# Kernel optimization log

Hardware: AMD Instinct MI355X
Metric: run time of the kernel (lower is better)

Reference implementation:

```python
import jax, jax.numpy as jnp
import numpy as np

EMBED_DIM = 1024
NUM_HEADS = 16
HEAD_DIM = EMBED_DIM // NUM_HEADS  # used only for the softmax scale


def setup_inputs() -> dict:
    key = jax.random.key(0)
    k_x, k_wqkv, k_bqkv, k_wo, k_bo = jax.random.split(key, 5)
    bound_qkv = 1.0 / np.sqrt(EMBED_DIM)
    return {
        "x": jax.random.normal(k_x, (4, 2048, EMBED_DIM), dtype=jnp.float32),
        "W_qkv": jax.random.uniform(k_wqkv, (EMBED_DIM, 3 * EMBED_DIM), jnp.float32, -bound_qkv, bound_qkv),
        "b_qkv": jax.random.uniform(k_bqkv, (3 * EMBED_DIM,), jnp.float32, -bound_qkv, bound_qkv),
        "W_out": jax.random.uniform(k_wo, (EMBED_DIM, EMBED_DIM), jnp.float32, -bound_qkv, bound_qkv),
        "b_out": jax.random.uniform(k_bo, (EMBED_DIM,), jnp.float32, -bound_qkv, bound_qkv),
    }


def reference(x, W_qkv, b_qkv, W_out, b_out):
    # fused QKV projection: [B,S,3E]
    qkv = jnp.einsum("bse,ef->bsf", x, W_qkv) + b_qkv
    q, k, v = jnp.split(qkv, 3, axis=-1)  # each [B,S,E]
    scale = 1.0 / jnp.sqrt(jnp.float32(HEAD_DIM))
    # NOTE: no head reshape — attention over full embed_dim, scale uses head_dim
    scores = jnp.einsum("bqe,bke->bqk", q, k) * scale  # [B,S,S]
    attn = jax.nn.softmax(scores, axis=-1)
    context = jnp.einsum("bqk,bke->bqe", attn, v)  # [B,S,E]
    return jnp.einsum("bse,ef->bsf", context, W_out) + b_out
```

## Files before the change

kernel.cpp:

```cpp
#include <hip/hip_runtime.h>

typedef unsigned short u16;
typedef __bf16   bf16x8 __attribute__((ext_vector_type(8)));
typedef float    f32x4  __attribute__((ext_vector_type(4)));
typedef unsigned short u16x4 __attribute__((ext_vector_type(4)));
typedef unsigned short u16x8 __attribute__((ext_vector_type(8)));

__device__ inline float bf2f(u16 u) { return __uint_as_float(((unsigned int)u) << 16); }
__device__ inline u16 f2bf(float f) {
    unsigned int u = __float_as_uint(f);
    u += 0x7FFF + ((u >> 16) & 1);
    return (u16)(u >> 16);
}

__device__ inline void gl2lds16(const u16* g, u16* l) {
    __builtin_amdgcn_global_load_lds(
        (const __attribute__((address_space(1))) void*)g,
        (__attribute__((address_space(3))) void*)l, 16, 0, 0);
}

__global__ __launch_bounds__(256)
void sniff_zero(const u16* __restrict__ x, int* __restrict__ flag,
                float* __restrict__ sums) {
    sums[blockIdx.x * 256 + threadIdx.x] = 0.0f;
    if (blockIdx.x == 0 && threadIdx.x < 64) {
        const int lane = threadIdx.x;
        const unsigned idx = lane * 131072u + 65536u;
        const u16 u = x[idx];
        const int e = (u >> 7) & 0xFF;
        const unsigned long long b = __ballot(e >= 100 && e <= 140);
        if (lane == 0) flag[0] = (__popcll(b) >= 48) ? 0 : 1;
    }
}

__global__ __launch_bounds__(256)
void convx_biases(const void* __restrict__ x, u16* __restrict__ xbf,
                  const void* __restrict__ b1, const void* __restrict__ b2,
                  u16* __restrict__ o1, u16* __restrict__ o2,
                  const int* __restrict__ flagp) {
    const int f = *flagp;
    if (blockIdx.x < 8192) {
        const long i = ((long)blockIdx.x * 256 + threadIdx.x) * 4;
        if (f) {
            f32x4 v = *(const f32x4*)((const float*)x + i);
            u16x4 o; o[0] = f2bf(v[0]); o[1] = f2bf(v[1]); o[2] = f2bf(v[2]); o[3] = f2bf(v[3]);
            *(u16x4*)(xbf + i) = o;
        } else {
            *(u16x4*)(xbf + i) = *(const u16x4*)((const u16*)x + i);
        }
    } else {
        const int i = (blockIdx.x - 8192) * 256 + threadIdx.x;
        if (i < 3072) o1[i] = f ? f2bf(((const float*)b1)[i]) : ((const u16*)b1)[i];
        else { const int j = i - 3072;
               o2[j] = f ? f2bf(((const float*)b2)[j]) : ((const u16*)b2)[j]; }
    }
}

__global__ __launch_bounds__(256)
void transpose_w(const void* __restrict__ Wqkv, u16* __restrict__ WqkvT,
                 const void* __restrict__ Wout, u16* __restrict__ WoutT,
                 const int* __restrict__ flagp)
{
    const void* in; u16* out; long inStride, outStride;
    if (blockIdx.z == 0) { in = Wqkv; out = WqkvT; inStride = 3072; outStride = 1024; }
    else { if (blockIdx.x >= 32) return;
           in = Wout; out = WoutT; inStride = 1024; outStride = 1024; }
    __shared__ u16 t[32][36];
    const int isF32 = *flagp;
    const int tid = threadIdx.x;
    const long r0 = (long)blockIdx.y * 32;
    const long c0 = (long)blockIdx.x * 32;
    const int r  = tid >> 3;
    const int c4 = (tid & 7) * 4;
    const long base = (r0 + r) * inStride + c0 + c4;
    u16x4 v;
    if (isF32) {
        f32x4 f = *(const f32x4*)((const float*)in + base);
        v[0] = f2bf(f[0]); v[1] = f2bf(f[1]); v[2] = f2bf(f[2]); v[3] = f2bf(f[3]);
    } else {
        v = *(const u16x4*)((const u16*)in + base);
    }
    t[r][c4 + 0] = v[0]; t[r][c4 + 1] = v[1]; t[r][c4 + 2] = v[2]; t[r][c4 + 3] = v[3];
    __syncthreads();
    u16x4 o;
    o[0] = t[c4 + 0][r]; o[1] = t[c4 + 1][r]; o[2] = t[c4 + 2][r]; o[3] = t[c4 + 3][r];
    *(u16x4*)&out[(c0 + r) * outStride + r0 + c4] = o;
}

template <int GM, int GN, int WM, int WN>
__device__ __forceinline__ void kloop(
    const u16* __restrict__ A, const u16* __restrict__ Bt,
    int K, long lda, long ldb, long m0, long n0,
    u16* __restrict__ As, u16* __restrict__ Bs, f32x4 (&acc)[WM][WN])
{
    constexpr int BM = GM * WM * 16;
    constexpr int BN = GN * WN * 16;
    constexpr int IA = BM / 32;
    constexpr int IB = BN / 32;
    const int tid  = threadIdx.x;
    const int lane = tid & 63;
    const int wave = tid >> 6;
    const int sr   = tid >> 3;
    const int qg0  = (tid & 7) ^ (sr & 7);
    const u16* pa[IA]; const u16* pb[IB];
    u16* la[IA]; u16* lb[IB];
#pragma unroll
    for (int i = 0; i < IA; ++i) {
        pa[i] = A + (m0 + i * 32 + sr) * lda + qg0 * 8;
        la[i] = As + (i * 256 + wave * 64) * 8;
    }
#pragma unroll
    for (int i = 0; i < IB; ++i) {
        pb[i] = Bt + (n0 + i * 32 + sr) * ldb + qg0 * 8;
        lb[i] = Bs + (i * 256 + wave * 64) * 8;
    }
    const int wm = (wave / GN) * (WM * 16);
    const int wn = (wave % GN) * (WN * 16);
    const int lr = lane & 15;
    const int hk = lane >> 4;
    int aoff[WM][2], boff[WN][2];
#pragma unroll
    for (int i = 0; i < WM; ++i) {
        const int row = wm + i * 16 + lr, r7 = row & 7;
        aoff[i][0] = row * 64 + ((hk     ^ r7) * 8);
        aoff[i][1] = row * 64 + (((4+hk) ^ r7) * 8);
    }
#pragma unroll
    for (int j = 0; j < WN; ++j) {
        const int row = wn + j * 16 + lr, r7 = row & 7;
        boff[j][0] = row * 64 + ((hk     ^ r7) * 8);
        boff[j][1] = row * 64 + (((4+hk) ^ r7) * 8);
    }
    for (int kt = 0; kt < K; kt += 64) {
#pragma unroll
        for (int i = 0; i < IA; ++i) { gl2lds16(pa[i], la[i]); pa[i] += 64; }
#pragma unroll
        for (int i = 0; i < IB; ++i) { gl2lds16(pb[i], lb[i]); pb[i] += 64; }
        __syncthreads();
#pragma unroll
        for (int ks = 0; ks < 2; ++ks) {
            bf16x8 af[WM], bf[WN];
#pragma unroll
            for (int i = 0; i < WM; ++i) af[i] = *(const bf16x8*)&As[aoff[i][ks]];
#pragma unroll
            for (int j = 0; j < WN; ++j) bf[j] = *(const bf16x8*)&Bs[boff[j][ks]];
#pragma unroll
            for (int i = 0; i < WM; ++i)
#pragma unroll
                for (int j = 0; j < WN; ++j)
                    acc[i][j] = __builtin_amdgcn_mfma_f32_16x16x32_bf16(af[i], bf[j], acc[i][j], 0, 0, 0);
        }
        __syncthreads();
    }
}

template <int WM, int WN, typename F>
__device__ __forceinline__ void epi_bf16(u16* __restrict__ Sw, u16* __restrict__ C,
    long ldc, long gm0, long gn0, int lane, F f)
{
    const int lr = lane & 15, hk = lane >> 4;
#pragma unroll
    for (int i = 0; i < WM; ++i)
#pragma unroll
        for (int j = 0; j < WN; ++j)
#pragma unroll
            for (int r = 0; r < 4; ++r)
                Sw[(i*16 + hk*4 + r) * (WN*16) + j*16 + lr] = f2bf(f(i, j, r));
    asm volatile("s_waitcnt lgkmcnt(0)" ::: "memory");
    constexpr int LPR = WN * 2;
    constexpr int RPI = 64 / LPR;
    const int rl = lane / LPR, c8 = (lane % LPR) * 8;
#pragma unroll
    for (int t = 0; t < (WM*16) / RPI; ++t) {
        const int row = t * RPI + rl;
        u16x8 v8 = *(const u16x8*)&Sw[row * (WN*16) + c8];
        *(u16x8*)&C[(gm0 + row) * ldc + gn0 + c8] = v8;
    }
}

template <int WM, int WN, typename F>
__device__ __forceinline__ void epi_f32(float* __restrict__ Sw, float* __restrict__ C,
    long ldc, long gm0, long gn0, int lane, F f)
{
    const int lr = lane & 15, hk = lane >> 4;
#pragma unroll
    for (int jh = 0; jh < 2; ++jh) {
#pragma unroll
        for (int i = 0; i < WM; ++i)
#pragma unroll
            for (int jj = 0; jj < WN/2; ++jj)
#pragma unroll
                for (int r = 0; r < 4; ++r)
                    Sw[(i*16 + hk*4 + r) * (WN*8) + jj*16 + lr] = f(i, jh*(WN/2) + jj, r);
        asm volatile("s_waitcnt lgkmcnt(0)" ::: "memory");
        constexpr int LPR = WN * 2;
        constexpr int RPI = 64 / LPR;
        const int rl = lane / LPR, c4 = (lane % LPR) * 4;
#pragma unroll
        for (int t = 0; t < (WM*16) / RPI; ++t) {
            const int row = t * RPI + rl;
            f32x4 v4 = *(const f32x4*)&Sw[row * (WN*8) + c4];
            *(f32x4*)&C[(gm0 + row) * ldc + gn0 + jh*(WN*8) + c4] = v4;
        }
        asm volatile("s_waitcnt lgkmcnt(0)" ::: "memory");
    }
}

__global__ __launch_bounds__(256, 4)
void gemm_qkv(const u16* __restrict__ A, const u16* __restrict__ Bt,
              u16* __restrict__ C, const u16* __restrict__ bias)
{
    __shared__ __align__(16) u16 S[256 * 64];
    const long m0 = (long)blockIdx.y * 128, n0 = (long)blockIdx.x * 128;
    f32x4 acc[4][4] = {};
    kloop<2, 2, 4, 4>(A, Bt, 1024, 1024L, 1024L, m0, n0, S, S + 128*64, acc);
    const int lane = threadIdx.x & 63, wave = threadIdx.x >> 6;
    const int wm = (wave >> 1) * 64, wn = (wave & 1) * 64;
    const int lr = lane & 15;
    float bj[4];
#pragma unroll
    for (int j = 0; j < 4; ++j) bj[j] = bf2f(bias[n0 + wn + j*16 + lr]);
    epi_bf16<4, 4>(S + wave * 4096, C, 3072L, m0 + wm, n0 + wn, lane,
        [&](int i, int j, int r) { return acc[i][j][r] + bj[j]; });
}

__global__ __launch_bounds__(256, 4)
void gemm_phase2(const u16* __restrict__ QKV, u16* __restrict__ P,
                 const u16* __restrict__ WoutT, u16* __restrict__ VWT,
                 float* __restrict__ sums)
{
    __shared__ __align__(16) u16 S[256 * 64];
    const int z = blockIdx.z;
    const u16 *Ap, *Bp; u16* Cp; long lda, ldb, ldc, m0, n0;
    bool doExp; float* srow = nullptr;
    if (z < 4) {
        const long zb = (long)z * 2048 * 3072;
        Ap = QKV + zb; Bp = QKV + 1024 + zb;
        Cp = P + (long)z * 2048 * 2048;
        lda = 3072; ldb = 3072; ldc = 2048;
        m0 = (long)blockIdx.y * 128; n0 = (long)blockIdx.x * 128;
        doExp = true; srow = sums + z * 2048;
    } else {
        const int vb = (z - 4) * 2 + (blockIdx.y >> 3);
        Ap = WoutT; lda = 1024;
        Bp = QKV + 2048 + (long)vb * 2048 * 3072; ldb = 3072;
        Cp = VWT + (long)vb * 1024 * 2048; ldc = 2048;
        m0 = (long)(blockIdx.y & 7) * 128; n0 = (long)blockIdx.x * 128;
        doExp = false;
    }
    f32x4 acc[4][4] = {};
    kloop<2, 2, 4, 4>(Ap, Bp, 1024, lda, ldb, m0, n0, S, S + 128*64, acc);
    const int lane = threadIdx.x & 63, wave = threadIdx.x >> 6;
    const int wm = (wave >> 1) * 64, wn = (wave & 1) * 64;
    const int lr = lane & 15, hk = lane >> 4;
    u16* Sw = S + wave * 4096;
    if (doExp) {
#pragma unroll
        for (int i = 0; i < 4; ++i)
#pragma unroll
            for (int r = 0; r < 4; ++r) {
                const int lrow = i*16 + hk*4 + r;
                float s = 0.0f;
#pragma unroll
                for (int j = 0; j < 4; ++j) {
                    const float e = __expf(acc[i][j][r] * 0.125f);
                    Sw[lrow * 64 + j*16 + lr] = f2bf(e);
                    s += e;
                }
                s += __shfl_xor(s, 1); s += __shfl_xor(s, 2);
                s += __shfl_xor(s, 4); s += __shfl_xor(s, 8);
                if (lr == 0) atomicAdd(&srow[m0 + wm + lrow], s);
            }
        asm volatile("s_waitcnt lgkmcnt(0)" ::: "memory");
        const int rl = lane >> 3, c8 = (lane & 7) * 8;
#pragma unroll
        for (int t = 0; t < 8; ++t) {
            const int row = t * 8 + rl;
            u16x8 v8 = *(const u16x8*)&Sw[row * 64 + c8];
            *(u16x8*)&Cp[(m0 + wm + row) * ldc + n0 + wn + c8] = v8;
        }
    } else {
        epi_bf16<4, 4>(Sw, Cp, ldc, m0 + wm, n0 + wn, lane,
            [&](int i, int j, int r) { return acc[i][j][r]; });
    }
}

__global__ __launch_bounds__(256, 4)
void gemm_final(const u16* __restrict__ P, const u16* __restrict__ VWT,
                void* __restrict__ out, const u16* __restrict__ bias,
                const float* __restrict__ sums, const int* __restrict__ flagp)
{
    __shared__ __align__(16) u16 S[256 * 64];
    const int outF32 = *flagp;
    const long bz = blockIdx.z;
    const long m0 = (long)blockIdx.y * 128, n0 = (long)blockIdx.x * 128;
    f32x4 acc[4][4] = {};
    kloop<2, 2, 4, 4>(P + bz * 2048 * 2048, VWT + bz * 1024 * 2048,
                      2048, 2048L, 2048L, m0, n0, S, S + 128*64, acc);
    const int lane = threadIdx.x & 63, wave = threadIdx.x >> 6;
    const int wm = (wave >> 1) * 64, wn = (wave & 1) * 64;
    const int lr = lane & 15, hk = lane >> 4;
    float inv[4][4], bj[4];
#pragma unroll
    for (int i = 0; i < 4; ++i)
#pragma unroll
        for (int r = 0; r < 4; ++r)
            inv[i][r] = 1.0f / sums[bz * 2048 + m0 + wm + i*16 + hk*4 + r];
#pragma unroll
    for (int j = 0; j < 4; ++j) bj[j] = bf2f(bias[n0 + wn + j*16 + lr]);
    if (outF32) {
        float* Co = (float*)out + bz * 2048 * 1024;
        epi_f32<4, 4>((float*)S + wave * 2048, Co, 1024L, m0 + wm, n0 + wn, lane,
            [&](int i, int j, int r) { return acc[i][j][r] * inv[i][r] + bj[j]; });
    } else {
        u16* Co = (u16*)out + bz * 2048 * 1024;
        epi_bf16<4, 4>(S + wave * 4096, Co, 1024L, m0 + wm, n0 + wn, lane,
            [&](int i, int j, int r) { return acc[i][j][r] * inv[i][r] + bj[j]; });
    }
}

extern "C" void kernel_launch(void* const* d_in, const int* in_sizes, int n_in,
                              void* d_out, int out_size, void* d_ws, size_t ws_size,
                              hipStream_t stream)
{
    const void* x    = d_in[0];
    const void* Wqkv = d_in[1];
    const void* bqkv = d_in[2];
    const void* Wout = d_in[3];
    const void* bout = d_in[4];
    char* ws = (char*)d_ws;

    u16*   xbf   = (u16*)(ws);
    u16*   WqkvT = (u16*)(ws + 16777216);
    u16*   P     = (u16*)(ws);
    u16*   QKV   = (u16*)(ws + 33554432);
    u16*   VWT   = (u16*)(ws + 83886080);
    u16*   WoutT = (u16*)(ws + 100663296);
    u16*   bqkvc = (u16*)(ws + 102760448);
    u16*   boutc = (u16*)(ws + 102766592);
    int*   flag  = (int*)(ws + 102768640);
    float* sums  = (float*)(ws + 102772736);

    dim3 blk(256);

    sniff_zero<<<32, blk, 0, stream>>>((const u16*)x, flag, sums);
    convx_biases<<<8208, blk, 0, stream>>>(x, xbf, bqkv, bout, bqkvc, boutc, flag);
    transpose_w<<<dim3(96, 32, 2), blk, 0, stream>>>(Wqkv, WqkvT, Wout, WoutT, flag);

    gemm_qkv<<<dim3(24, 64, 1), blk, 0, stream>>>(xbf, WqkvT, QKV, bqkvc);

    gemm_phase2<<<dim3(16, 16, 6), blk, 0, stream>>>(QKV, P, WoutT, VWT, sums);

    gemm_final<<<dim3(8, 16, 4), blk, 0, stream>>>(P, VWT, d_out, boutc, sums, flag);
}
```

Measured before the change: 267.3 us.

## Use 256x256 tiles with 8-wave four-phase pipelined k-loop for QKV and phase2 GEMMs

Replaces the 128x128, 4-wave GEMM kernels for the QKV projection and the scores/V·Wout stage with 256x256 tiles on 512-thread blocks. The new k-loop splits each 64-wide k-step into four quarter phases that interleave direct global-to-LDS loads of the next tile with MFMA work, and raises wave priority during the MFMAs. The goal is better operand reuse per byte loaded and hiding load latency. The cost is 128 KB of LDS per block and fewer blocks per CU, and a 256-row tile grid that may fill the GPU's CUs less evenly.

```diff
diff --git a/kernel.cpp b/kernel.cpp
--- a/kernel.cpp
+++ b/kernel.cpp
@@ -206,30 +206,152 @@
     }
 }
 
-__global__ __launch_bounds__(256, 4)
-void gemm_qkv(const u16* __restrict__ A, const u16* __restrict__ Bt,
-              u16* __restrict__ C, const u16* __restrict__ bias)
-{
-    __shared__ __align__(16) u16 S[256 * 64];
-    const long m0 = (long)blockIdx.y * 128, n0 = (long)blockIdx.x * 128;
-    f32x4 acc[4][4] = {};
-    kloop<2, 2, 4, 4>(A, Bt, 1024, 1024L, 1024L, m0, n0, S, S + 128*64, acc);
+template<int MH, int NH, typename FI>
+__device__ __forceinline__ void phase256(const u16* Ab, const u16* Bb,
+    int aB0, int aB1, int bB0, int bB1, f32x4 (&acc)[2][2][4][2], FI issue)
+{
+    bf16x8 af[2][4], bv[2][2];
+#pragma unroll
+    for (int i = 0; i < 4; ++i) {
+        af[0][i] = *(const bf16x8*)&Ab[aB0 + MH*8192 + i*1024];
+        af[1][i] = *(const bf16x8*)&Ab[aB1 + MH*8192 + i*1024];
+    }
+#pragma unroll
+    for (int j = 0; j < 2; ++j) {
+        bv[0][j] = *(const bf16x8*)&Bb[bB0 + NH*8192 + j*1024];
+        bv[1][j] = *(const bf16x8*)&Bb[bB1 + NH*8192 + j*1024];
+    }
+    issue();
+    __builtin_amdgcn_s_barrier();
+    asm volatile("s_waitcnt lgkmcnt(0)" ::: "memory");
+    __builtin_amdgcn_s_setprio(1);
+#pragma unroll
+    for (int ks = 0; ks < 2; ++ks)
+#pragma unroll
+        for (int i = 0; i < 4; ++i)
+#pragma unroll
+            for (int j = 0; j < 2; ++j)
+                acc[MH][NH][i][j] = __builtin_amdgcn_mfma_f32_16x16x32_bf16(
+                    af[ks][i], bv[ks][j], acc[MH][NH][i][j], 0, 0, 0);
+    __builtin_amdgcn_s_setprio(0);
+}
+
+__device__ __forceinline__ void kloop256(
+    const u16* __restrict__ A, const u16* __restrict__ Bt,
+    int K, long lda, long ldb, long m0, long n0,
+    u16* __restrict__ S, f32x4 (&acc)[2][2][4][2])
+{
+    constexpr int BUF = 256 * 64;
+    const int tid  = threadIdx.x;
+    const int wave = tid >> 6, lane = tid & 63;
+    const int wmi  = wave >> 2, wni = wave & 3;
+    const int sr   = tid >> 3;
+    const int qg   = ((tid & 7) ^ (sr & 7)) * 8;
+    const int lr   = lane & 15, hk = lane >> 4, l7 = lane & 7;
+    const u16* pA = A + (m0 + sr) * lda + qg;
+    const u16* pB = Bt + (n0 + sr) * ldb + qg;
+    u16* const lA = S + wave * 512;
+    u16* const lB = S + 2 * BUF + wave * 512;
+    const int aB0 = (wmi*64 + lr)*64 + ((hk       ^ l7) * 8);
+    const int aB1 = (wmi*64 + lr)*64 + (((4 + hk) ^ l7) * 8);
+    const int bB0 = (wni*32 + lr)*64 + ((hk       ^ l7) * 8);
+    const int bB1 = (wni*32 + lr)*64 + (((4 + hk) ^ l7) * 8);
+    const int NT = K >> 6;
+
+    auto stA = [&](int buf, int mh, int kt) {
+        const u16* s = pA + (long)mh * 128 * lda + kt;
+        u16* d = lA + buf * BUF + mh * 8192;
+        gl2lds16(s, d);
+        gl2lds16(s + 64 * lda, d + 4096);
+    };
+    auto stB = [&](int buf, int nh, int kt) {
+        const u16* s = pB + (long)nh * 128 * ldb + kt;
+        u16* d = lB + buf * BUF + nh * 8192;
+        gl2lds16(s, d);
+        gl2lds16(s + 64 * ldb, d + 4096);
+    };
+
+    stA(0, 0, 0); stB(0, 0, 0); stA(0, 1, 0); stB(0, 1, 0);
+    stA(1, 0, 64); stB(1, 0, 64);
+    asm volatile("s_waitcnt vmcnt(4)" ::: "memory");
+    __builtin_amdgcn_s_barrier();
+
+    for (int t = 0; t < NT; ++t) {
+        const int b = t & 1;
+        const u16* Ab = S + b * BUF;
+        const u16* Bb = S + 2 * BUF + b * BUF;
+        const int kt = t << 6;
+        phase256<0,0>(Ab, Bb, aB0, aB1, bB0, bB1, acc,
+                      [&]{ if (t + 1 < NT) stA(b ^ 1, 1, kt + 64); });
+        __builtin_amdgcn_s_barrier();
+        phase256<0,1>(Ab, Bb, aB0, aB1, bB0, bB1, acc,
+                      [&]{ if (t + 1 < NT) stB(b ^ 1, 1, kt + 64); });
+        __builtin_amdgcn_s_barrier();
+        phase256<1,0>(Ab, Bb, aB0, aB1, bB0, bB1, acc,
+                      [&]{ if (t + 2 < NT) stA(b, 0, kt + 128); });
+        __builtin_amdgcn_s_barrier();
+        phase256<1,1>(Ab, Bb, aB0, aB1, bB0, bB1, acc,
+                      [&]{ if (t + 2 < NT) stB(b, 0, kt + 128); });
+        if (t + 2 < NT)      asm volatile("s_waitcnt vmcnt(4)" ::: "memory");
+        else if (t + 1 < NT) asm volatile("s_waitcnt vmcnt(0)" ::: "memory");
+        __builtin_amdgcn_s_barrier();
+    }
+}
+
+template <typename F>
+__device__ __forceinline__ void epi256_bf16(u16* __restrict__ Sw, u16* __restrict__ C,
+    long ldc, long m0, long n0, int wmi, int wni, int lane, F f)
+{
+    const int lr = lane & 15, hk = lane >> 4;
+#pragma unroll
+    for (int mh = 0; mh < 2; ++mh)
+#pragma unroll
+    for (int i = 0; i < 4; ++i)
+#pragma unroll
+    for (int r = 0; r < 4; ++r)
+#pragma unroll
+    for (int nh = 0; nh < 2; ++nh)
+#pragma unroll
+    for (int j = 0; j < 2; ++j)
+        Sw[(mh*64 + i*16 + hk*4 + r) * 64 + nh*32 + j*16 + lr] = f2bf(f(mh, nh, i, j, r));
+    asm volatile("s_waitcnt lgkmcnt(0)" ::: "memory");
+    const int rl = lane >> 3, c8 = (lane & 7) * 8;
+    const long gcolb = n0 + (long)((c8 >> 5) * 128 + wni * 32 + (c8 & 31));
+#pragma unroll
+    for (int t = 0; t < 16; ++t) {
+        const int row = t * 8 + rl;
+        const long grow = m0 + (row >> 6) * 128 + wmi * 64 + (row & 63);
+        *(u16x8*)&C[grow * ldc + gcolb] = *(const u16x8*)&Sw[row * 64 + c8];
+    }
+}
+
+__global__ __launch_bounds__(512, 2)
+void gemm_qkv256(const u16* __restrict__ A, const u16* __restrict__ Bt,
+                 u16* __restrict__ C, const u16* __restrict__ bias)
+{
+    __shared__ __align__(16) u16 S[65536];
+    const long m0 = (long)blockIdx.y * 256, n0 = (long)blockIdx.x * 256;
+    f32x4 acc[2][2][4][2] = {};
+    kloop256(A, Bt, 1024, 1024L, 1024L, m0, n0, S, acc);
     const int lane = threadIdx.x & 63, wave = threadIdx.x >> 6;
-    const int wm = (wave >> 1) * 64, wn = (wave & 1) * 64;
+    const int wmi = wave >> 2, wni = wave & 3;
     const int lr = lane & 15;
-    float bj[4];
-#pragma unroll
-    for (int j = 0; j < 4; ++j) bj[j] = bf2f(bias[n0 + wn + j*16 + lr]);
-    epi_bf16<4, 4>(S + wave * 4096, C, 3072L, m0 + wm, n0 + wn, lane,
-        [&](int i, int j, int r) { return acc[i][j][r] + bj[j]; });
-}
-
-__global__ __launch_bounds__(256, 4)
-void gemm_phase2(const u16* __restrict__ QKV, u16* __restrict__ P,
-                 const u16* __restrict__ WoutT, u16* __restrict__ VWT,
-                 float* __restrict__ sums)
-{
-    __shared__ __align__(16) u16 S[256 * 64];
+    float bj[2][2];
+#pragma unroll
+    for (int nh = 0; nh < 2; ++nh)
+#pragma unroll
+        for (int j = 0; j < 2; ++j)
+            bj[nh][j] = bf2f(bias[n0 + nh*128 + wni*32 + j*16 + lr]);
+    epi256_bf16(S + wave * 8192, C, 3072L, m0, n0, wmi, wni, lane,
+        [&](int mh, int nh, int i, int j, int r) { return acc[mh][nh][i][j][r] + bj[nh][j]; });
+}
+
+__global__ __launch_bounds__(512, 2)
+void gemm_phase2_256(const u16* __restrict__ QKV, u16* __restrict__ P,
+                     const u16* __restrict__ WoutT, u16* __restrict__ VWT,
+                     float* __restrict__ sums)
+{
+    __shared__ __align__(16) u16 S[65536];
     const int z = blockIdx.z;
     const u16 *Ap, *Bp; u16* Cp; long lda, ldb, ldc, m0, n0;
     bool doExp; float* srow = nullptr;
@@ -238,50 +360,54 @@
         Ap = QKV + zb; Bp = QKV + 1024 + zb;
         Cp = P + (long)z * 2048 * 2048;
         lda = 3072; ldb = 3072; ldc = 2048;
-        m0 = (long)blockIdx.y * 128; n0 = (long)blockIdx.x * 128;
+        m0 = (long)blockIdx.y * 256; n0 = (long)blockIdx.x * 256;
         doExp = true; srow = sums + z * 2048;
     } else {
-        const int vb = (z - 4) * 2 + (blockIdx.y >> 3);
+        const int vb = (z - 4) * 2 + (blockIdx.y >> 2);
         Ap = WoutT; lda = 1024;
         Bp = QKV + 2048 + (long)vb * 2048 * 3072; ldb = 3072;
         Cp = VWT + (long)vb * 1024 * 2048; ldc = 2048;
-        m0 = (long)(blockIdx.y & 7) * 128; n0 = (long)blockIdx.x * 128;
+        m0 = (long)(blockIdx.y & 3) * 256; n0 = (long)blockIdx.x * 256;
         doExp = false;
     }
-    f32x4 acc[4][4] = {};
-    kloop<2, 2, 4, 4>(Ap, Bp, 1024, lda, ldb, m0, n0, S, S + 128*64, acc);
+    f32x4 acc[2][2][4][2] = {};
+    kloop256(Ap, Bp, 1024, lda, ldb, m0, n0, S, acc);
     const int lane = threadIdx.x & 63, wave = threadIdx.x >> 6;
-    const int wm = (wave >> 1) * 64, wn = (wave & 1) * 64;
+    const int wmi = wave >> 2, wni = wave & 3;
     const int lr = lane & 15, hk = lane >> 4;
-    u16* Sw = S + wave * 4096;
+    u16* Sw = S + wave * 8192;
     if (doExp) {
 #pragma unroll
+        for (int mh = 0; mh < 2; ++mh)
+#pragma unroll
         for (int i = 0; i < 4; ++i)
 #pragma unroll
-            for (int r = 0; r < 4; ++r) {
-                const int lrow = i*16 + hk*4 + r;
-                float s = 0.0f;
-#pragma unroll
-                for (int j = 0; j < 4; ++j) {
-                    const float e = __expf(acc[i][j][r] * 0.125f);
-                    Sw[lrow * 64 + j*16 + lr] = f2bf(e);
-                    s += e;
-                }
-                s += __shfl_xor(s, 1); s += __shfl_xor(s, 2);
-                s += __shfl_xor(s, 4); s += __shfl_xor(s, 8);
-                if (lr == 0) atomicAdd(&srow[m0 + wm + lrow], s);
+        for (int r = 0; r < 4; ++r) {
+            float s = 0.0f;
+#pragma unroll
+            for (int nh = 0; nh < 2; ++nh)
+#pragma unroll
+            for (int j = 0; j < 2; ++j) {
+                const float e = __expf(acc[mh][nh][i][j][r] * 0.125f);
+                Sw[(mh*64 + i*16 + hk*4 + r) * 64 + nh*32 + j*16 + lr] = f2bf(e);
+                s += e;
             }
+            s += __shfl_xor(s, 1); s += __shfl_xor(s, 2);
+            s += __shfl_xor(s, 4); s += __shfl_xor(s, 8);
+            if (lr == 0) atomicAdd(&srow[m0 + mh*128 + wmi*64 + i*16 + hk*4 + r], s);
+        }
         asm volatile("s_waitcnt lgkmcnt(0)" ::: "memory");
         const int rl = lane >> 3, c8 = (lane & 7) * 8;
-#pragma unroll
-        for (int t = 0; t < 8; ++t) {
+        const long gcolb = n0 + (long)((c8 >> 5) * 128 + wni * 32 + (c8 & 31));
+#pragma unroll
+        for (int t = 0; t < 16; ++t) {
             const int row = t * 8 + rl;
-            u16x8 v8 = *(const u16x8*)&Sw[row * 64 + c8];
-            *(u16x8*)&Cp[(m0 + wm + row) * ldc + n0 + wn + c8] = v8;
+            const long grow = m0 + (row >> 6) * 128 + wmi * 64 + (row & 63);
+            *(u16x8*)&Cp[grow * ldc + gcolb] = *(const u16x8*)&Sw[row * 64 + c8];
         }
     } else {
-        epi_bf16<4, 4>(Sw, Cp, ldc, m0 + wm, n0 + wn, lane,
-            [&](int i, int j, int r) { return acc[i][j][r]; });
+        epi256_bf16(Sw, Cp, ldc, m0, n0, wmi, wni, lane,
+            [&](int mh, int nh, int i, int j, int r) { return acc[mh][nh][i][j][r]; });
     }
 }
 
@@ -347,9 +473,9 @@
     convx_biases<<<8208, blk, 0, stream>>>(x, xbf, bqkv, bout, bqkvc, boutc, flag);
     transpose_w<<<dim3(96, 32, 2), blk, 0, stream>>>(Wqkv, WqkvT, Wout, WoutT, flag);
 
-    gemm_qkv<<<dim3(24, 64, 1), blk, 0, stream>>>(xbf, WqkvT, QKV, bqkvc);
-
-    gemm_phase2<<<dim3(16, 16, 6), blk, 0, stream>>>(QKV, P, WoutT, VWT, sums);
+    gemm_qkv256<<<dim3(12, 32, 1), dim3(512), 0, stream>>>(xbf, WqkvT, QKV, bqkvc);
+
+    gemm_phase2_256<<<dim3(8, 8, 6), dim3(512), 0, stream>>>(QKV, P, WoutT, VWT, sums);
 
     gemm_final<<<dim3(8, 16, 4), blk, 0, stream>>>(P, VWT, d_out, boutc, sums, flag);
 }
```

Result: slower. 304.1 us (+13.8%).
